# Kernel optimization log

Hardware: AMD Instinct MI355X
Metric: run time of the kernel (lower is better)

The kernel has to match this reference:

```python
import jax, jax.numpy as jnp
import numpy as np

B, N, H, NH = 8, 1024, 768, 12
AS = H // NH
SCALE = AS ** -0.5
NEG_SLOPE = 0.02  # LeakyReLU(0.02)
M = 256           # occurrence pairs per batch item


def _lin(k, out_d, in_d):
    k1, k2 = jax.random.split(k)
    w = jax.random.normal(k1, (out_d, in_d), jnp.float32) * (in_d ** -0.5)
    b = jax.random.normal(k2, (out_d,), jnp.float32) * 0.01
    return w, b


def setup_inputs():
    key = jax.random.key(0)
    ks = jax.random.split(key, 10)
    W_var, b_var = _lin(ks[0], H, H)
    W_sym, b_sym = _lin(ks[1], H, H)
    W_score, b_score = _lin(ks[2], 1, 2 * H)
    W_cross, b_cross = _lin(ks[3], 1, H)
    W_atom, b_atom = _lin(ks[4], H, 2 * H)
    W_q, b_q = _lin(ks[5], H, H)
    W_k, b_k = _lin(ks[6], H, H)
    W_v, b_v = _lin(ks[7], H, H)
    W_o, b_o = _lin(ks[8], H, H)
    x = jax.random.normal(ks[9], (B, N, H), jnp.float32)
    # predicates every 3rd node starting at 2 (no overlapping writes, i+1 < N)
    pp = np.zeros((B, N), np.int32)
    pp[:, 2:N - 2:3] = 1
    rng = np.random.default_rng(0)
    occ = np.stack([rng.permutation(N)[:2 * M].reshape(M, 2) for _ in range(B)]).astype(np.int32)
    return dict(
        x=x,
        atom_graph=jnp.zeros((B, N, N), jnp.float32),
        variable_graph=jnp.zeros((B, N, N), jnp.float32),
        W_var=W_var, b_var=b_var, W_sym=W_sym, b_sym=b_sym,
        W_score=W_score, b_score=b_score, W_cross=W_cross, b_cross=b_cross,
        W_atom=W_atom, b_atom=b_atom, W_q=W_q, b_q=b_q, W_k=W_k, b_k=b_k,
        W_v=W_v, b_v=b_v, W_o=W_o, b_o=b_o,
        predicate_pos=jnp.asarray(pp),
        variable_tags=jnp.zeros((B, N), jnp.int32),
        attention_mask=jnp.ones((B, N), jnp.int32),
        occurrence_list=jnp.asarray(occ),
    )


def reference(x, atom_graph, variable_graph,
              W_var, b_var, W_sym, b_sym, W_score, b_score, W_cross, b_cross,
              W_atom, b_atom, W_q, b_q, W_k, b_k, W_v, b_v, W_o, b_o,
              predicate_pos, variable_tags, attention_mask, occurrence_list):
    lrelu = lambda v: jax.nn.leaky_relu(v, NEG_SLOPE)
    idx = jnp.arange(N)
    pred = predicate_pos == 1                              # [B,N]
    pp_prev2 = jnp.roll(predicate_pos, 2, axis=1)          # pp[i-2]
    # branch: single-neighbor var (i==0 or pp[i-2]==1) vs averaged neighbors
    single = (idx[None, :] == 0) | ((idx[None, :] >= 2) & (pp_prev2 == 1))
    x_prev = jnp.roll(x, 1, axis=1)
    x_next = jnp.roll(x, -1, axis=1)
    var_in = jnp.where(single[..., None], x_next, (x_prev + x_next) * 0.5)
    var_feat = var_in @ W_var.T + b_var
    sym_feat = x @ W_sym.T + b_sym
    t = jnp.tanh(jnp.concatenate([var_feat, sym_feat], axis=-1))
    s = lrelu(t @ W_score.T + b_score)[..., 0]             # [B,N] edge scores
    # write masks: (i-1,i)/(i,i-1) for preds i>=1; (i,i+1)/(i+1,i) for i<=1 or double branch
    lower = pred & (idx[None, :] >= 1)
    upper = pred & ((idx[None, :] <= 1) | ~single)
    sl = jnp.where(lower, s, 0.0)
    su = jnp.where(upper, s, 0.0)
    im1 = jnp.clip(idx - 1, 0, N - 1)
    ip1 = jnp.clip(idx + 1, 0, N - 1)
    AG = atom_graph
    AG = AG.at[:, im1, idx].add(sl).at[:, idx, im1].add(sl)
    AG = AG.at[:, idx, ip1].add(su).at[:, ip1, idx].add(su)
    # variable (cross-atom occurrence) graph
    o0, o1 = occurrence_list[..., 0], occurrence_list[..., 1]
    barange = jnp.arange(B)[:, None]
    xm = (x[barange, o0] + x[barange, o1]) * 0.5           # [B,M,H]
    sc = lrelu(xm @ W_cross.T + b_cross)[..., 0]           # [B,M]
    VG = variable_graph.at[barange, o0, o1].add(sc).at[barange, o1, o0].add(sc)
    # multi-head attention with graph biases
    q = (x @ W_q.T + b_q).reshape(B, N, NH, AS).transpose(0, 2, 1, 3) * SCALE
    k = (x @ W_k.T + b_k).reshape(B, N, NH, AS).transpose(0, 2, 1, 3)
    v = (x @ W_v.T + b_v).reshape(B, N, NH, AS).transpose(0, 2, 1, 3)
    att = jnp.einsum('bhnd,bhmd->bhnm', q, k)
    AG = 0.2 * AG + 0.8 * (AG @ AG)
    VG2 = VG @ VG
    att = att + AG[:, None] + VG2[:, None]
    att = jax.nn.softmax(att, axis=-1)                     # dropout omitted (eval)
    y = jnp.einsum('bhnm,bhmd->bhnd', att, v).transpose(0, 2, 1, 3).reshape(B, N, H)
    y = y @ W_o.T + b_o
    # path embedding: weighted mean of per-predicate atom embeds (weight 2 or 3)
    y_prev = jnp.roll(y, 1, axis=1)
    y_next = jnp.roll(y, -1, axis=1)
    var_y = jnp.where(single[..., None], y_next, (y_prev + y_next) * 0.5)
    atom = jnp.concatenate([var_y, y], axis=-1) @ W_atom.T + b_atom  # [B,N,H]
    triple = upper & (idx[None, :] >= 1)
    w = jnp.where(pred, jnp.where(triple, 3.0, 2.0), 0.0)
    pm = (w[..., None] * atom).sum(axis=1) / w.sum(axis=1)[:, None]  # [B,H]
    return jnp.broadcast_to(pm[:, None, :], (B, N, H))
```

## Files before the change

### kernel.cpp

```cpp
#include <hip/hip_runtime.h>
#include <hip/hip_bf16.h>

#define BB 8
#define NN 1024
#define HH 768
#define NHD 12
#define ASZ 64
#define MM 256
#define QSCALE 0.125f
#define NSLOPE 0.02f
#define LOG2E 1.44269504f
#define PRMAX 384

typedef __attribute__((ext_vector_type(8))) short bf16x8;
typedef __attribute__((ext_vector_type(4))) float f32x4;

#define EXP2F(x) __builtin_amdgcn_exp2f(x)
#define RCPF(x)  __builtin_amdgcn_rcpf(x)

#define OFFB_QB    ((size_t)0)
#define OFFB_KB    ((size_t)12582912)
#define OFFB_VB    ((size_t)25165824)
#define OFFB_XB    ((size_t)37748736)
#define OFFB_WQB   ((size_t)50331648)
#define OFFB_WKB   ((size_t)51511296)
#define OFFB_WVB   ((size_t)52690944)
#define OFFB_WVAR  ((size_t)53870592)
#define OFFB_WSYM  ((size_t)55050240)
#define OFFB_SRAW  ((size_t)56229888)
#define OFFB_DIAG  ((size_t)56262656)
#define OFFB_BIAS4 ((size_t)56295424)
#define OFFB_PLIST ((size_t)56426496)
#define OFFB_PCNT  ((size_t)56459264)
#define OFFB_SUMW  ((size_t)56459296)
#define OFFB_ZZ    ((size_t)56459328)
#define OFFB_TV    ((size_t)56508480)
#define OFFB_PM    ((size_t)56557632)
#define OFFB_VROWS ((size_t)56582208)

__device__ __forceinline__ float lrelu(float v) { return v >= 0.f ? v : NSLOPE * v; }

__device__ __forceinline__ ushort f2bf(float f) {
  return (ushort)((__float_as_uint(f) + 0x8000u) >> 16);
}
__device__ __forceinline__ float bf2f(ushort u) {
  union { unsigned u; float f; } v; v.u = (unsigned)u << 16;
  return v.f;
}
__device__ __forceinline__ unsigned packbf2(float lo, float hi) {
  unsigned a = __float_as_uint(hi) + 0x8000u;
  unsigned b = __float_as_uint(lo) + 0x8000u;
  return __builtin_amdgcn_perm(a, b, 0x07060302u);
}
__device__ __forceinline__ float fast_tanh(float x) {
  float e = EXP2F(x * (2.f * LOG2E));
  return 1.f - 2.f * RCPF(e + 1.f);
}

__device__ __forceinline__ void coefs(const int* ppb, int j, float& c1, float& c2) {
  auto pred = [&](int tt) { return tt >= 0 && tt < NN && ppb[tt] == 1; };
  auto single = [&](int tt) { return tt == 0 || (tt >= 2 && ppb[tt - 2] == 1); };
  auto wgt = [&](int tt) {
    if (!pred(tt)) return 0.f;
    bool tri = (tt >= 1) && (tt <= 1 || !single(tt));
    return tri ? 3.f : 2.f;
  };
  float a = 0.f;
  if (pred(j + 1)) a += wgt(j + 1) * (single(j + 1) ? 0.f : 0.5f);
  if (j >= 1 && pred(j - 1)) a += wgt(j - 1) * (single(j - 1) ? 1.f : 0.5f);
  c1 = a;
  c2 = wgt(j);
}

__global__ void k_cvt(const float* __restrict__ src, ushort* __restrict__ dst, int n4) {
  int i = blockIdx.x * 256 + threadIdx.x;
  if (i >= n4) return;
  float4 v = ((const float4*)src)[i];
  ushort4 o;
  o.x = f2bf(v.x); o.y = f2bf(v.y); o.z = f2bf(v.z); o.w = f2bf(v.w);
  ((ushort4*)dst)[i] = o;
}

__global__ void k_cvt5(const float* __restrict__ s0, const float* __restrict__ s1,
                       const float* __restrict__ s2, const float* __restrict__ s3,
                       const float* __restrict__ s4,
                       ushort* __restrict__ d0, ushort* __restrict__ d1,
                       ushort* __restrict__ d2, ushort* __restrict__ d3,
                       ushort* __restrict__ d4) {
  int z = blockIdx.y;
  const float* src = z == 0 ? s0 : z == 1 ? s1 : z == 2 ? s2 : z == 3 ? s3 : s4;
  ushort* dst = z == 0 ? d0 : z == 1 ? d1 : z == 2 ? d2 : z == 3 ? d3 : d4;
  int i = blockIdx.x * 256 + threadIdx.x;
  float4 v = ((const float4*)src)[i];
  ushort4 o;
  o.x = f2bf(v.x); o.y = f2bf(v.y); o.z = f2bf(v.z); o.w = f2bf(v.w);
  ((ushort4*)dst)[i] = o;
}

__global__ void k_pred(const int* __restrict__ pp, int* __restrict__ plist,
                       int* __restrict__ pcnt, float* __restrict__ sumw,
                       float* __restrict__ sraw, float* __restrict__ diag,
                       float* __restrict__ zz) {
  int b = blockIdx.x;
  int lane = threadIdx.x;
  const int* ppb = pp + b * NN;
  int base = 0;
  float wacc = 0.f;
  for (int c = 0; c < NN; c += 64) {
    int i = c + lane;
    bool isp = ppb[i] == 1;
    unsigned long long mask = __ballot(isp);
    if (isp) {
      int pos = base + __popcll(mask & ((1ull << lane) - 1ull));
      plist[b * NN + pos] = i;
      bool sing = (i == 0) || (i >= 2 && ppb[i - 2] == 1);
      bool tri = (i >= 1) && (i <= 1 || !sing);
      wacc += tri ? 3.f : 2.f;
    }
    base += __popcll(mask);
  }
  for (int off = 32; off; off >>= 1) wacc += __shfl_xor(wacc, off);
  if (lane == 0) { pcnt[b] = base; sumw[b] = wacc; }
  for (int c = lane; c < NN; c += 64) { sraw[b * NN + c] = 0.f; diag[b * NN + c] = 0.f; }
  for (int c = lane; c < HH; c += 64) {
    zz[b * HH + c] = 0.f;
    zz[BB * HH + b * HH + c] = 0.f;
  }
}

__global__ void k_gather(const ushort* __restrict__ xb, const int* __restrict__ pp,
                         const int* __restrict__ plist, const int* __restrict__ pcnt,
                         ushort* __restrict__ vrows) {
  int b = blockIdx.y;
  int j = blockIdx.x * 4 + (threadIdx.x >> 6);
  int lane = threadIdx.x & 63;
  if (j >= pcnt[b]) return;
  int i = plist[b * NN + j];
  bool sing = (i == 0) || (i >= 2 && pp[b * NN + i - 2] == 1);
  float wa = sing ? 0.f : 0.5f, wb = sing ? 1.f : 0.5f;
  const ushort* rp = xb + (size_t)(b * NN + ((i - 1) & (NN - 1))) * HH;
  const ushort* rn = xb + (size_t)(b * NN + ((i + 1) & (NN - 1))) * HH;
  ushort* dst = vrows + ((size_t)b * PRMAX + j) * HH;
#pragma unroll
  for (int it = 0; it < 3; ++it) {
    int d4 = lane + it * 64;
    ushort4 p4 = ((const ushort4*)rp)[d4];
    ushort4 n4 = ((const ushort4*)rn)[d4];
    ushort4 o;
    o.x = f2bf(wa * bf2f(p4.x) + wb * bf2f(n4.x));
    o.y = f2bf(wa * bf2f(p4.y) + wb * bf2f(n4.y));
    o.z = f2bf(wa * bf2f(p4.z) + wb * bf2f(n4.z));
    o.w = f2bf(wa * bf2f(p4.w) + wb * bf2f(n4.w));
    ((ushort4*)dst)[d4] = o;
  }
}

__global__ void k_cross(const float* __restrict__ x, const int* __restrict__ occ,
                        const float* __restrict__ Wc, const float* __restrict__ bc,
                        float* __restrict__ diag) {
  int g = blockIdx.x * 4 + (threadIdx.x >> 6);
  int lane = threadIdx.x & 63;
  int b = g >> 8, m = g & (MM - 1);
  int o0 = occ[(b * MM + m) * 2 + 0];
  int o1 = occ[(b * MM + m) * 2 + 1];
  const float* x0 = x + (size_t)(b * NN + o0) * HH;
  const float* x1 = x + (size_t)(b * NN + o1) * HH;
  float acc = 0.f;
  for (int d = lane; d < HH; d += 64) acc += 0.5f * (x0[d] + x1[d]) * Wc[d];
  for (int off = 32; off; off >>= 1) acc += __shfl_xor(acc, off);
  if (lane == 0) {
    float sc = lrelu(acc + bc[0]);
    float sq = sc * sc;
    diag[b * NN + o0] = sq;
    diag[b * NN + o1] = sq;
  }
}

__global__ __launch_bounds__(256, 2) void k_score_mf(
    const ushort* __restrict__ xb, const ushort* __restrict__ vrows,
    const int* __restrict__ plist, const int* __restrict__ pcnt,
    const ushort* __restrict__ Wvar, const ushort* __restrict__ Wsym,
    const float* __restrict__ bvar, const float* __restrict__ bsym,
    const float* __restrict__ wscore, float* __restrict__ s_raw) {
  const int b = blockIdx.z;
  const int cnt = pcnt[b];
  const int j0 = blockIdx.y * 64;
  if (j0 >= cnt) return;
  const int n0g = blockIdx.x * 128;
  const bool symh = n0g >= HH;
  const int n0 = symh ? n0g - HH : n0g;
  const ushort* W = symh ? Wsym : Wvar;
  const float* bias = symh ? bsym : bvar;
  __shared__ ushort As[64 * 64];
  __shared__ ushort Bs[128 * 64];
  __shared__ int pl[64];
  __shared__ float red[64];
  const int t = threadIdx.x;
  const int w = t >> 6, lane = t & 63, lg = lane >> 4, lm = lane & 15;
  const int wm = (w >> 1) * 32, wn = (w & 1) * 64;
  if (t < 64) {
    int j = j0 + t;
    pl[t] = (j < cnt) ? plist[b * NN + j] : 2;
    red[t] = 0.f;
  }
  __syncthreads();
  const int r0 = t >> 3, c = t & 7;
  const ushort* ap0; const ushort* ap1;
  if (symh) {
    const ushort* xbb = xb + (size_t)b * NN * HH;
    ap0 = xbb + (size_t)pl[r0] * HH + c * 8;
    ap1 = xbb + (size_t)pl[r0 + 32] * HH + c * 8;
  } else {
    const ushort* vrb = vrows + ((size_t)b * PRMAX + j0) * HH;
    ap0 = vrb + (size_t)r0 * HH + c * 8;
    ap1 = vrb + (size_t)(r0 + 32) * HH + c * 8;
  }
  const ushort* bp = W + (size_t)(n0 + r0) * HH + c * 8;
  uint4 ar0 = *(const uint4*)ap0;
  uint4 ar1 = *(const uint4*)ap1;
  uint4 br0 = *(const uint4*)bp;
  uint4 br1 = *(const uint4*)(bp + (size_t)32 * HH);
  uint4 br2 = *(const uint4*)(bp + (size_t)64 * HH);
  uint4 br3 = *(const uint4*)(bp + (size_t)96 * HH);
  f32x4 acc[2][4] = {};
  const int ssw = (c ^ (r0 & 7)) * 8;
  for (int k0 = 0; k0 < HH; k0 += 64) {
    if (k0) __syncthreads();
    *(uint4*)&As[r0 * 64 + ssw] = ar0;
    *(uint4*)&As[(r0 + 32) * 64 + ssw] = ar1;
    *(uint4*)&Bs[r0 * 64 + ssw] = br0;
    *(uint4*)&Bs[(r0 + 32) * 64 + ssw] = br1;
    *(uint4*)&Bs[(r0 + 64) * 64 + ssw] = br2;
    *(uint4*)&Bs[(r0 + 96) * 64 + ssw] = br3;
    __syncthreads();
    if (k0 + 64 < HH) {
      ap0 += 64; ap1 += 64; bp += 64;
      ar0 = *(const uint4*)ap0;
      ar1 = *(const uint4*)ap1;
      br0 = *(const uint4*)bp;
      br1 = *(const uint4*)(bp + (size_t)32 * HH);
      br2 = *(const uint4*)(bp + (size_t)64 * HH);
      br3 = *(const uint4*)(bp + (size_t)96 * HH);
    }
    bf16x8 af[2][2], bfr[4][2];
#pragma unroll
    for (int mt = 0; mt < 2; ++mt)
#pragma unroll
      for (int kt = 0; kt < 2; ++kt) {
        int row = wm + mt * 16 + lm, ch = lg + kt * 4;
        af[mt][kt] = *(bf16x8*)&As[row * 64 + ((ch ^ (row & 7)) * 8)];
      }
#pragma unroll
    for (int nt = 0; nt < 4; ++nt)
#pragma unroll
      for (int kt = 0; kt < 2; ++kt) {
        int row = wn + nt * 16 + lm, ch = lg + kt * 4;
        bfr[nt][kt] = *(bf16x8*)&Bs[row * 64 + ((ch ^ (row & 7)) * 8)];
      }
#pragma unroll
    for (int mt = 0; mt < 2; ++mt)
#pragma unroll
      for (int nt = 0; nt < 4; ++nt)
#pragma unroll
        for (int kt = 0; kt < 2; ++kt)
          acc[mt][nt] = __builtin_amdgcn_mfma_f32_16x16x32_bf16(af[mt][kt], bfr[nt][kt], acc[mt][nt], 0, 0, 0);
  }
  float bcol[4], wcol[4];
#pragma unroll
  for (int nt = 0; nt < 4; ++nt) {
    int cl = wn + nt * 16 + lm;
    bcol[nt] = bias[n0 + cl];
    wcol[nt] = wscore[n0g + cl];
  }
#pragma unroll
  for (int mt = 0; mt < 2; ++mt)
#pragma unroll
    for (int r = 0; r < 4; ++r) {
      float p = 0.f;
#pragma unroll
      for (int nt = 0; nt < 4; ++nt)
        p += fast_tanh(acc[mt][nt][r] + bcol[nt]) * wcol[nt];
      p += __shfl_xor(p, 1); p += __shfl_xor(p, 2);
      p += __shfl_xor(p, 4); p += __shfl_xor(p, 8);
      if (lm == 0) atomicAdd(&red[wm + mt * 16 + lg * 4 + r], p);
    }
  __syncthreads();
  if (t < 64) {
    int j2 = j0 + t;
    if (j2 < cnt) atomicAdd(&s_raw[b * NN + pl[t]], red[t]);
  }
}

__global__ void k_bias(const int* __restrict__ pp, const float* __restrict__ s_raw,
                       const float* __restrict__ diag, const float* __restrict__ b_score,
                       float4* __restrict__ bias4) {
  int g = blockIdx.x * 256 + threadIdx.x;
  int b = g >> 10, r = g & (NN - 1);
  const int* ppb = pp + b * NN;
  int i = -1;
  if (ppb[r] == 1) i = r;
  else if (r + 1 < NN && ppb[r + 1] == 1) i = r + 1;
  else if (r >= 1 && ppb[r - 1] == 1) i = r - 1;
  float v0 = 0.f, v1 = 0.f, v2 = 0.f; int cw = r;
  if (i >= 1 && i + 1 < NN) {
    float s = lrelu(s_raw[b * NN + i] + b_score[0]);
    float s2 = s * s;
    cw = i - 1;
    if (i == r) { v0 = 0.2f * s; v1 = 1.6f * s2; v2 = 0.2f * s; }
    else       { v0 = 0.8f * s2; v1 = 0.2f * s; v2 = 0.8f * s2; }
  }
  int slot = r - cw;
  float d = diag[g];
  if (slot == 0) v0 += d; else if (slot == 1) v1 += d; else v2 += d;
  bias4[g] = make_float4(__int_as_float(cw), v0 * LOG2E, v1 * LOG2E, v2 * LOG2E);
}

__global__ __launch_bounds__(256, 2) void k_gemm_bf(
    const ushort* __restrict__ X,
    const ushort* __restrict__ W0, const ushort* __restrict__ W1, const ushort* __restrict__ W2,
    const float* __restrict__ b0, const float* __restrict__ b1, const float* __restrict__ b2,
    ushort* __restrict__ C0, ushort* __restrict__ C1, ushort* __restrict__ C2) {
  const int z = blockIdx.z;
  const ushort* W = z == 0 ? W0 : (z == 1 ? W1 : W2);
  const float* bias = z == 0 ? b0 : (z == 1 ? b1 : b2);
  ushort* C = z == 0 ? C0 : (z == 1 ? C1 : C2);
  const float alpha = z == 0 ? QSCALE * LOG2E : 1.f;
  __shared__ ushort As[128 * 64];
  __shared__ ushort Bs[128 * 64];
  const int m0 = blockIdx.x * 128, n0 = blockIdx.y * 128;
  const int t = threadIdx.x;
  const int w = t >> 6, lane = t & 63, lg = lane >> 4, lm = lane & 15;
  const int wm = (w >> 1) * 64, wn = (w & 1) * 64;
  f32x4 acc[4][4] = {};
  for (int k0 = 0; k0 < HH; k0 += 64) {
    __syncthreads();
#pragma unroll
    for (int it = 0; it < 4; ++it) {
      int slot = t + it * 256;
      int row = slot >> 3, c = slot & 7;
      uint4 va = *(const uint4*)(X + (size_t)(m0 + row) * HH + k0 + c * 8);
      *(uint4*)&As[row * 64 + ((c ^ (row & 7)) * 8)] = va;
      uint4 vb = *(const uint4*)(W + (size_t)(n0 + row) * HH + k0 + c * 8);
      *(uint4*)&Bs[row * 64 + ((c ^ (row & 7)) * 8)] = vb;
    }
    __syncthreads();
    bf16x8 af[4][2], bfr[4][2];
#pragma unroll
    for (int mt = 0; mt < 4; ++mt)
#pragma unroll
      for (int kt = 0; kt < 2; ++kt) {
        int row = wm + mt * 16 + lm, ch = lg + kt * 4;
        af[mt][kt] = *(bf16x8*)&As[row * 64 + ((ch ^ (row & 7)) * 8)];
      }
#pragma unroll
    for (int nt = 0; nt < 4; ++nt)
#pragma unroll
      for (int kt = 0; kt < 2; ++kt) {
        int row = wn + nt * 16 + lm, ch = lg + kt * 4;
        bfr[nt][kt] = *(bf16x8*)&Bs[row * 64 + ((ch ^ (row & 7)) * 8)];
      }
#pragma unroll
    for (int mt = 0; mt < 4; ++mt)
#pragma unroll
      for (int nt = 0; nt < 4; ++nt)
#pragma unroll
        for (int kt = 0; kt < 2; ++kt)
          acc[mt][nt] = __builtin_amdgcn_mfma_f32_16x16x32_bf16(af[mt][kt], bfr[nt][kt], acc[mt][nt], 0, 0, 0);
  }
  if (z == 2) {
#pragma unroll
    for (int nt = 0; nt < 4; ++nt) {
      int col = n0 + wn + nt * 16 + lm;
      int hh = col >> 6, dd = col & 63;
      float bcol = bias[col];
#pragma unroll
      for (int mt = 0; mt < 4; ++mt) {
        int row0 = m0 + wm + mt * 16 + lg * 4;
        int bb2 = row0 >> 10, nr = row0 & (NN - 1);
        ushort4 o;
        o.x = f2bf(acc[mt][nt][0] + bcol);
        o.y = f2bf(acc[mt][nt][1] + bcol);
        o.z = f2bf(acc[mt][nt][2] + bcol);
        o.w = f2bf(acc[mt][nt][3] + bcol);
        *(ushort4*)(C + ((size_t)(bb2 * NHD + hh) * ASZ + dd) * NN + nr) = o;
      }
    }
  } else {
#pragma unroll
    for (int nt = 0; nt < 4; ++nt) {
      int col = n0 + wn + nt * 16 + lm;
      float bcol = bias[col];
#pragma unroll
      for (int mt = 0; mt < 4; ++mt)
#pragma unroll
        for (int r = 0; r < 4; ++r) {
          int row = m0 + wm + mt * 16 + lg * 4 + r;
          C[(size_t)row * HH + col] = f2bf((acc[mt][nt][r] + bcol) * alpha);
        }
    }
  }
}

__global__ __launch_bounds__(512, 2) void k_attn2(
    const ushort* __restrict__ qg, const ushort* __restrict__ kg, const ushort* __restrict__ vtg,
    const float4* __restrict__ bias4, const int* __restrict__ pp, float* __restrict__ zz) {
  __shared__ ushort Ks[64 * 64];
  __shared__ ushort Vts[64 * 64];
  const int rb = blockIdx.y, h = blockIdx.x >> 3, b = blockIdx.x & 7;
  const int n0 = rb * 128;
  const int t = threadIdx.x, w = t >> 6, lane = t & 63, lg = lane >> 4, lm = lane & 15;
  const int qbase = n0 + w * 16;
  const ushort* qrow = qg + (size_t)(b * NN + qbase + lm) * HH + h * ASZ;
  bf16x8 qf[2];
  qf[0] = *(const bf16x8*)(qrow + lg * 8);
  qf[1] = *(const bf16x8*)(qrow + lg * 8 + 32);
  float4 bz = bias4[b * NN + qbase + lm];
  const int cwq = __float_as_int(bz.x);
  float mr = -1e30f, lr = 0.f;
  f32x4 y[4] = {};
  const ushort* kb = kg + (size_t)(b * NN) * HH + h * ASZ;
  const ushort* vtb = vtg + (size_t)(b * NHD + h) * ASZ * NN;
  const int srow = t >> 3, sc = t & 7;
  const int arow = (srow & 35) | ((srow & 4) << 2) | ((srow & 24) >> 1);
  const ushort* kptr = kb + (size_t)srow * HH + sc * 8;
  const ushort* vptr = vtb + (size_t)srow * NN + sc * 8;
  uint4 kreg = *(const uint4*)kptr;
  uint4 vreg = *(const uint4*)vptr;
  for (int tile = 0; tile < 16; ++tile) {
    const int c0 = tile * 64;
    *(uint4*)&Ks[arow * 64 + ((sc ^ (arow & 7)) * 8)] = kreg;
    *(uint4*)&Vts[srow * 64 + ((sc ^ (srow & 7)) * 8)] = vreg;
    __syncthreads();
    if (tile < 15) {
      kptr += 64 * HH; vptr += 64;
      kreg = *(const uint4*)kptr;
      vreg = *(const uint4*)vptr;
    }
    f32x4 s[4] = {};
#pragma unroll
    for (int nt = 0; nt < 4; ++nt) {
      int krow = lm + nt * 16, sw = krow & 7;
#pragma unroll
      for (int kt = 0; kt < 2; ++kt) {
        bf16x8 kf = *(bf16x8*)&Ks[krow * 64 + (((lg + kt * 4) ^ sw) * 8)];
        s[nt] = __builtin_amdgcn_mfma_f32_16x16x32_bf16(kf, qf[kt], s[nt], 0, 0, 0);
      }
    }
    if (c0 <= qbase + 17 && qbase <= c0 + 65) {
#pragma unroll
      for (int nt = 0; nt < 4; ++nt) {
        int kb2 = c0 + (nt >> 1) * 32 + lg * 8 + (nt & 1) * 4;
#pragma unroll
        for (int r = 0; r < 4; ++r) {
          int dd = kb2 + r - cwq;
          if (dd >= 0 && dd < 3) s[nt][r] += (dd == 0) ? bz.y : (dd == 1 ? bz.z : bz.w);
        }
      }
    }
    f32x4 m4;
#pragma unroll
    for (int e = 0; e < 4; ++e)
      m4[e] = fmaxf(fmaxf(s[0][e], s[1][e]), fmaxf(s[2][e], s[3][e]));
    float tm = fmaxf(fmaxf(m4[0], m4[1]), fmaxf(m4[2], m4[3]));
    tm = fmaxf(tm, __shfl_xor(tm, 16));
    tm = fmaxf(tm, __shfl_xor(tm, 32));
    int need = tm > mr;
    if (__any(need)) {
      float mn = fmaxf(mr, tm);
      float f = EXP2F(mr - mn);
      mr = mn;
      lr *= f;
      float fr[4];
#pragma unroll
      for (int r = 0; r < 4; ++r) fr[r] = __shfl(f, lg * 4 + r);
#pragma unroll
      for (int nt = 0; nt < 4; ++nt)
#pragma unroll
        for (int r = 0; r < 4; ++r) y[nt][r] *= fr[r];
    }
    f32x4 sum4 = {0.f, 0.f, 0.f, 0.f};
#pragma unroll
    for (int nt = 0; nt < 4; ++nt)
#pragma unroll
      for (int e = 0; e < 4; ++e) {
        float p = EXP2F(s[nt][e] - mr);
        s[nt][e] = p;
        sum4[e] += p;
      }
    float ts = (sum4[0] + sum4[1]) + (sum4[2] + sum4[3]);
    ts += __shfl_xor(ts, 16);
    ts += __shfl_xor(ts, 32);
    lr += ts;
    union { unsigned u[4]; bf16x8 v; } pk[2];
#pragma unroll
    for (int kt = 0; kt < 2; ++kt) {
      pk[kt].u[0] = packbf2(s[2 * kt][0], s[2 * kt][1]);
      pk[kt].u[1] = packbf2(s[2 * kt][2], s[2 * kt][3]);
      pk[kt].u[2] = packbf2(s[2 * kt + 1][0], s[2 * kt + 1][1]);
      pk[kt].u[3] = packbf2(s[2 * kt + 1][2], s[2 * kt + 1][3]);
    }
#pragma unroll
    for (int nt = 0; nt < 4; ++nt) {
      int vrow = lm + nt * 16, sw = vrow & 7;
#pragma unroll
      for (int kt = 0; kt < 2; ++kt) {
        bf16x8 vf = *(bf16x8*)&Vts[vrow * 64 + (((lg + kt * 4) ^ sw) * 8)];
        y[nt] = __builtin_amdgcn_mfma_f32_16x16x32_bf16(pk[kt].v, vf, y[nt], 0, 0, 0);
      }
    }
    __syncthreads();
  }
  float invl = 1.f / lr;
  float invq[4], c1v[4], c2v[4];
#pragma unroll
  for (int r = 0; r < 4; ++r) {
    invq[r] = __shfl(invl, lg * 4 + r);
    coefs(pp + b * NN, qbase + lg * 4 + r, c1v[r], c2v[r]);
  }
  float a1[4], a2[4];
#pragma unroll
  for (int nt = 0; nt < 4; ++nt) {
    float u1 = 0.f, u2 = 0.f;
#pragma unroll
    for (int r = 0; r < 4; ++r) {
      float yv = y[nt][r] * invq[r];
      u1 += c1v[r] * yv;
      u2 += c2v[r] * yv;
    }
    u1 += __shfl_xor(u1, 16); u1 += __shfl_xor(u1, 32);
    u2 += __shfl_xor(u2, 16); u2 += __shfl_xor(u2, 32);
    a1[nt] = u1; a2[nt] = u2;
  }
  if (lg == 0) {
#pragma unroll
    for (int nt = 0; nt < 4; ++nt) {
      atomicAdd(&zz[b * HH + h * ASZ + nt * 16 + lm], a1[nt]);
      atomicAdd(&zz[BB * HH + b * HH + h * ASZ + nt * 16 + lm], a2[nt]);
    }
  }
}

__global__ void k_f1(const float* __restrict__ Wo, const float* __restrict__ bo,
                     const float* __restrict__ zz, const float* __restrict__ sumw,
                     float* __restrict__ tvec) {
  int b = blockIdx.y;
  int w = threadIdx.x >> 6, lane = threadIdx.x & 63;
  float inv = 1.f / sumw[b];
  const float* z1 = zz + b * HH;
  const float* z2 = zz + BB * HH + b * HH;
  float zr1[12], zr2[12];
#pragma unroll
  for (int m = 0; m < 12; ++m) { zr1[m] = z1[lane + 64 * m] * inv; zr2[m] = z2[lane + 64 * m] * inv; }
  for (int j = 0; j < 8; ++j) {
    int o = blockIdx.x * 32 + w * 8 + j;
    const float* wrow = Wo + (size_t)o * HH;
    float a1 = 0.f, a2 = 0.f;
#pragma unroll
    for (int m = 0; m < 12; ++m) { float wv = wrow[lane + 64 * m]; a1 += wv * zr1[m]; a2 += wv * zr2[m]; }
    for (int mask = 32; mask; mask >>= 1) { a1 += __shfl_xor(a1, mask); a2 += __shfl_xor(a2, mask); }
    if (lane == 0) { tvec[b * HH + o] = a1 + bo[o]; tvec[BB * HH + b * HH + o] = a2 + bo[o]; }
  }
}

__global__ void k_f2(const float* __restrict__ Wa, const float* __restrict__ ba,
                     const float* __restrict__ tvec, float* __restrict__ pm) {
  int b = blockIdx.y;
  int w = threadIdx.x >> 6, lane = threadIdx.x & 63;
  const float* t1 = tvec + b * HH;
  const float* t2 = tvec + BB * HH + b * HH;
  float r1[12], r2[12];
#pragma unroll
  for (int m = 0; m < 12; ++m) { r1[m] = t1[lane + 64 * m]; r2[m] = t2[lane + 64 * m]; }
  for (int j = 0; j < 8; ++j) {
    int o = blockIdx.x * 32 + w * 8 + j;
    const float* wrow = Wa + (size_t)o * (2 * HH);
    float a = 0.f;
#pragma unroll
    for (int m = 0; m < 12; ++m) a += wrow[lane + 64 * m] * r1[m];
#pragma unroll
    for (int m = 0; m < 12; ++m) a += wrow[HH + lane + 64 * m] * r2[m];
    for (int mask = 32; mask; mask >>= 1) a += __shfl_xor(a, mask);
    if (lane == 0) pm[b * HH + o] = a + ba[o];
  }
}

__global__ void k_bcast(const float* __restrict__ pm, float* __restrict__ out) {
  size_t g = (size_t)blockIdx.x * 256 + threadIdx.x;
  int b = (int)(g / ((size_t)NN * HH / 4));
  int hh4 = (int)(g % (HH / 4));
  float4 val = *(const float4*)(pm + b * HH + hh4 * 4);
  *(float4*)(out + g * 4) = val;
}

extern "C" void kernel_launch(void* const* d_in, const int* in_sizes, int n_in,
                              void* d_out, int out_size, void* d_ws, size_t ws_size,
                              hipStream_t stream) {
  (void)in_sizes; (void)n_in; (void)out_size; (void)ws_size;
  const float* x       = (const float*)d_in[0];
  const float* W_var   = (const float*)d_in[3];
  const float* b_var   = (const float*)d_in[4];
  const float* W_sym   = (const float*)d_in[5];
  const float* b_sym   = (const float*)d_in[6];
  const float* W_score = (const float*)d_in[7];
  const float* b_score = (const float*)d_in[8];
  const float* W_cross = (const float*)d_in[9];
  const float* b_cross = (const float*)d_in[10];
  const float* W_atom  = (const float*)d_in[11];
  const float* b_atom  = (const float*)d_in[12];
  const float* W_q     = (const float*)d_in[13];
  const float* b_q     = (const float*)d_in[14];
  const float* W_k     = (const float*)d_in[15];
  const float* b_k     = (const float*)d_in[16];
  const float* W_v     = (const float*)d_in[17];
  const float* b_v     = (const float*)d_in[18];
  const float* W_o     = (const float*)d_in[19];
  const float* b_o     = (const float*)d_in[20];
  const int*   pp      = (const int*)d_in[21];
  const int*   occ     = (const int*)d_in[24];
  float* out = (float*)d_out;
  char* wsb = (char*)d_ws;
  ushort* qb  = (ushort*)(wsb + OFFB_QB);
  ushort* kbf = (ushort*)(wsb + OFFB_KB);
  ushort* vtb = (ushort*)(wsb + OFFB_VB);
  ushort* xb  = (ushort*)(wsb + OFFB_XB);
  ushort* wqb = (ushort*)(wsb + OFFB_WQB);
  ushort* wkb = (ushort*)(wsb + OFFB_WKB);
  ushort* wvb = (ushort*)(wsb + OFFB_WVB);
  ushort* wvar = (ushort*)(wsb + OFFB_WVAR);
  ushort* wsym = (ushort*)(wsb + OFFB_WSYM);
  ushort* vrows = (ushort*)(wsb + OFFB_VROWS);
  float* sraw = (float*)(wsb + OFFB_SRAW);
  float* diag = (float*)(wsb + OFFB_DIAG);
  float4* bias4 = (float4*)(wsb + OFFB_BIAS4);
  int* plist = (int*)(wsb + OFFB_PLIST);
  int* pcnt  = (int*)(wsb + OFFB_PCNT);
  float* sumw = (float*)(wsb + OFFB_SUMW);
  float* zz   = (float*)(wsb + OFFB_ZZ);
  float* tv   = (float*)(wsb + OFFB_TV);
  float* pm   = (float*)(wsb + OFFB_PM);

  k_pred<<<BB, 64, 0, stream>>>(pp, plist, pcnt, sumw, sraw, diag, zz);
  k_cvt<<<(BB * NN * HH / 4 + 255) / 256, 256, 0, stream>>>(x, xb, BB * NN * HH / 4);
  k_cvt5<<<dim3(HH * HH / 4 / 256, 5), 256, 0, stream>>>(W_q, W_k, W_v, W_var, W_sym,
                                                          wqb, wkb, wvb, wvar, wsym);
  k_gather<<<dim3(PRMAX / 4, BB), 256, 0, stream>>>(xb, pp, plist, pcnt, vrows);
  k_score_mf<<<dim3(12, 6, BB), 256, 0, stream>>>(xb, vrows, plist, pcnt, wvar, wsym,
                                                  b_var, b_sym, W_score, sraw);
  k_cross<<<BB * MM / 4, 256, 0, stream>>>(x, occ, W_cross, b_cross, diag);
  k_bias<<<BB * NN / 256, 256, 0, stream>>>(pp, sraw, diag, b_score, bias4);
  k_gemm_bf<<<dim3(64, 6, 3), 256, 0, stream>>>(xb, wqb, wkb, wvb, b_q, b_k, b_v, qb, kbf, vtb);
  k_attn2<<<dim3(NHD * BB, NN / 128), 512, 0, stream>>>(qb, kbf, vtb, bias4, pp, zz);
  k_f1<<<dim3(24, BB), 256, 0, stream>>>(W_o, b_o, zz, sumw, tv);
  k_f2<<<dim3(24, BB), 256, 0, stream>>>(W_atom, b_atom, tv, pm);
  k_bcast<<<BB * NN * HH / 1024, 256, 0, stream>>>(pm, out);
}
```

Before: 172.4 us.

## Prefetch GEMM tiles into registers and double-buffer attention K/V LDS

The projection GEMM now loads the next K-slice of X and W into registers while the current slice is being multiplied, so global load latency overlaps the MFMA work. The attention kernel gets two LDS buffers for K and V^T: the next tile is written into the alternate buffer while the current one is consumed, leaving one barrier per iteration. This costs more registers in the GEMM and doubles the attention kernel's LDS use, which could reduce occupancy.

```diff
diff --git a/kernel.cpp b/kernel.cpp
--- a/kernel.cpp
+++ b/kernel.cpp
@@ -331,19 +331,41 @@
   const int t = threadIdx.x;
   const int w = t >> 6, lane = t & 63, lg = lane >> 4, lm = lane & 15;
   const int wm = (w >> 1) * 64, wn = (w & 1) * 64;
+  const int r0 = t >> 3, c = t & 7;
+  const int ssw = (c ^ (r0 & 7)) * 8;
+  const ushort* Xp = X + (size_t)(m0 + r0) * HH + c * 8;
+  const ushort* Wp = W + (size_t)(n0 + r0) * HH + c * 8;
+  uint4 xa0 = *(const uint4*)Xp;
+  uint4 xa1 = *(const uint4*)(Xp + (size_t)32 * HH);
+  uint4 xa2 = *(const uint4*)(Xp + (size_t)64 * HH);
+  uint4 xa3 = *(const uint4*)(Xp + (size_t)96 * HH);
+  uint4 wb0 = *(const uint4*)Wp;
+  uint4 wb1 = *(const uint4*)(Wp + (size_t)32 * HH);
+  uint4 wb2 = *(const uint4*)(Wp + (size_t)64 * HH);
+  uint4 wb3 = *(const uint4*)(Wp + (size_t)96 * HH);
   f32x4 acc[4][4] = {};
   for (int k0 = 0; k0 < HH; k0 += 64) {
+    if (k0) __syncthreads();
+    *(uint4*)&As[r0 * 64 + ssw] = xa0;
+    *(uint4*)&As[(r0 + 32) * 64 + ssw] = xa1;
+    *(uint4*)&As[(r0 + 64) * 64 + ssw] = xa2;
+    *(uint4*)&As[(r0 + 96) * 64 + ssw] = xa3;
+    *(uint4*)&Bs[r0 * 64 + ssw] = wb0;
+    *(uint4*)&Bs[(r0 + 32) * 64 + ssw] = wb1;
+    *(uint4*)&Bs[(r0 + 64) * 64 + ssw] = wb2;
+    *(uint4*)&Bs[(r0 + 96) * 64 + ssw] = wb3;
     __syncthreads();
-#pragma unroll
-    for (int it = 0; it < 4; ++it) {
-      int slot = t + it * 256;
-      int row = slot >> 3, c = slot & 7;
-      uint4 va = *(const uint4*)(X + (size_t)(m0 + row) * HH + k0 + c * 8);
-      *(uint4*)&As[row * 64 + ((c ^ (row & 7)) * 8)] = va;
-      uint4 vb = *(const uint4*)(W + (size_t)(n0 + row) * HH + k0 + c * 8);
-      *(uint4*)&Bs[row * 64 + ((c ^ (row & 7)) * 8)] = vb;
-    }
-    __syncthreads();
+    if (k0 + 64 < HH) {
+      Xp += 64; Wp += 64;
+      xa0 = *(const uint4*)Xp;
+      xa1 = *(const uint4*)(Xp + (size_t)32 * HH);
+      xa2 = *(const uint4*)(Xp + (size_t)64 * HH);
+      xa3 = *(const uint4*)(Xp + (size_t)96 * HH);
+      wb0 = *(const uint4*)Wp;
+      wb1 = *(const uint4*)(Wp + (size_t)32 * HH);
+      wb2 = *(const uint4*)(Wp + (size_t)64 * HH);
+      wb3 = *(const uint4*)(Wp + (size_t)96 * HH);
+    }
     bf16x8 af[4][2], bfr[4][2];
 #pragma unroll
     for (int mt = 0; mt < 4; ++mt)
@@ -404,8 +426,8 @@
 __global__ __launch_bounds__(512, 2) void k_attn2(
     const ushort* __restrict__ qg, const ushort* __restrict__ kg, const ushort* __restrict__ vtg,
     const float4* __restrict__ bias4, const int* __restrict__ pp, float* __restrict__ zz) {
-  __shared__ ushort Ks[64 * 64];
-  __shared__ ushort Vts[64 * 64];
+  __shared__ ushort Ks[2][64 * 64];
+  __shared__ ushort Vts[2][64 * 64];
   const int rb = blockIdx.y, h = blockIdx.x >> 3, b = blockIdx.x & 7;
   const int n0 = rb * 128;
   const int t = threadIdx.x, w = t >> 6, lane = t & 63, lg = lane >> 4, lm = lane & 15;
@@ -422,16 +444,26 @@
   const ushort* vtb = vtg + (size_t)(b * NHD + h) * ASZ * NN;
   const int srow = t >> 3, sc = t & 7;
   const int arow = (srow & 35) | ((srow & 4) << 2) | ((srow & 24) >> 1);
+  const int kssw = (sc ^ (arow & 7)) * 8;
+  const int vssw = (sc ^ (srow & 7)) * 8;
   const ushort* kptr = kb + (size_t)srow * HH + sc * 8;
   const ushort* vptr = vtb + (size_t)srow * NN + sc * 8;
   uint4 kreg = *(const uint4*)kptr;
   uint4 vreg = *(const uint4*)vptr;
+  *(uint4*)&Ks[0][arow * 64 + kssw] = kreg;
+  *(uint4*)&Vts[0][srow * 64 + vssw] = vreg;
+  kptr += 64 * HH; vptr += 64;
+  kreg = *(const uint4*)kptr;
+  vreg = *(const uint4*)vptr;
+  __syncthreads();
   for (int tile = 0; tile < 16; ++tile) {
     const int c0 = tile * 64;
-    *(uint4*)&Ks[arow * 64 + ((sc ^ (arow & 7)) * 8)] = kreg;
-    *(uint4*)&Vts[srow * 64 + ((sc ^ (srow & 7)) * 8)] = vreg;
-    __syncthreads();
+    const int cur = tile & 1;
     if (tile < 15) {
+      *(uint4*)&Ks[cur ^ 1][arow * 64 + kssw] = kreg;
+      *(uint4*)&Vts[cur ^ 1][srow * 64 + vssw] = vreg;
+    }
+    if (tile < 14) {
       kptr += 64 * HH; vptr += 64;
       kreg = *(const uint4*)kptr;
       vreg = *(const uint4*)vptr;
@@ -442,7 +474,7 @@
       int krow = lm + nt * 16, sw = krow & 7;
 #pragma unroll
       for (int kt = 0; kt < 2; ++kt) {
-        bf16x8 kf = *(bf16x8*)&Ks[krow * 64 + (((lg + kt * 4) ^ sw) * 8)];
+        bf16x8 kf = *(bf16x8*)&Ks[cur][krow * 64 + (((lg + kt * 4) ^ sw) * 8)];
         s[nt] = __builtin_amdgcn_mfma_f32_16x16x32_bf16(kf, qf[kt], s[nt], 0, 0, 0);
       }
     }
@@ -504,7 +536,7 @@
       int vrow = lm + nt * 16, sw = vrow & 7;
 #pragma unroll
       for (int kt = 0; kt < 2; ++kt) {
-        bf16x8 vf = *(bf16x8*)&Vts[vrow * 64 + (((lg + kt * 4) ^ sw) * 8)];
+        bf16x8 vf = *(bf16x8*)&Vts[cur][vrow * 64 + (((lg + kt * 4) ^ sw) * 8)];
         y[nt] = __builtin_amdgcn_mfma_f32_16x16x32_bf16(pk[kt].v, vf, y[nt], 0, 0, 0);
       }
     }
```

After: 168.4 us. 1.02x faster.
